# Kernel optimization log

Measured on AMD Instinct MI355X. Metric: run time of the kernel, lower is better.

The kernel has to match this reference:

```python
import jax, jax.numpy as jnp
import numpy as np

B, D, DM, K, KA = 4096, 64, 256, 32, 16


def setup_inputs() -> dict:
    key = jax.random.key(0)
    ks = jax.random.split(key, 20)
    rn = lambda i, shape, s=1.0: jax.random.normal(ks[i], shape, dtype=jnp.float32) * s
    return dict(
        z=rn(0, (B, D)),
        rw=jax.random.uniform(ks[1], (B, K), dtype=jnp.float32),
        action_z=rn(2, (B, D)),
        action_rw=jax.random.uniform(ks[3], (B, KA), dtype=jnp.float32),
        action_code_z=rn(4, (B, D)),
        control=rn(5, (B, D)),
        exact_covector=rn(6, (B, D)),
        chart_emb=rn(7, (K, DM), 0.05),
        chart_anchor=rn(8, (K, D)),
        action_chart_emb=rn(9, (KA, DM), 0.05),
        action_chart_anchor=rn(10, (KA, D)),
        z_embed_W=rn(11, (D, DM), 0.05), z_embed_b=jnp.zeros((DM,), jnp.float32),
        lat_W=rn(12, (D, DM), 0.05), lat_b=jnp.zeros((DM,), jnp.float32),
        code_W=rn(13, (D, DM), 0.05), code_b=jnp.zeros((DM,), jnp.float32),
        Wq=rn(14, (DM, DM), 0.05), Wk=rn(15, (DM, DM), 0.05),
        Wv=rn(16, (DM, DM), 0.05), Wo=rn(17, (DM, DM), 0.05),
        form_W=rn(18, (DM, D), 0.05), form_b=jnp.zeros((D,), jnp.float32),
    )


def _spectral_linear(x, W, b):
    # SpectralLinear: weight normalized by its largest singular value.
    sigma = jnp.linalg.svd(W, compute_uv=False)[0]
    return x @ (W / jnp.maximum(sigma, jnp.float32(1e-8))) + b


def _forward(z, rw, action_z, action_rw, action_code_z, control, exact_covector,
             chart_emb, chart_anchor, action_chart_emb, action_chart_anchor,
             z_embed_W, z_embed_b, lat_W, lat_b, code_W, code_b,
             Wq, Wk, Wv, Wo, form_W, form_b):
    b = z.shape[0]
    # ChartTokenizer: routing-weighted chart embeddings + anchor latents.
    chart_x = rw[:, :, None] * chart_emb[None]                      # [B,K,DM]
    chart_z = jnp.broadcast_to(chart_anchor[None], (b, K, D))       # [B,K,D]
    a_chart_x = action_rw[:, :, None] * action_chart_emb[None]      # [B,KA,DM]
    a_chart_z = jnp.broadcast_to(action_chart_anchor[None], (b, KA, D))
    # LatentTokenizers: single token per latent.
    lat_x = (action_z @ lat_W + lat_b)[:, None, :]                  # [B,1,DM]
    code_x = (action_code_z @ code_W + code_b)[:, None, :]          # [B,1,DM]
    ctx_x = jnp.concatenate([lat_x, code_x, a_chart_x, chart_x], axis=1)   # [B,S,DM]
    ctx_z = jnp.concatenate([action_z[:, None], action_code_z[:, None], a_chart_z, chart_z], axis=1)  # [B,S,D]
    # CovariantAttention (1 head): feature scores biased by latent-space distance.
    x_q = z @ z_embed_W + z_embed_b                                 # [B,DM]
    q = x_q @ Wq                                                    # [B,DM]
    k = jnp.einsum('bsd,de->bse', ctx_x, Wk)                        # [B,S,DM]
    v = jnp.einsum('bsd,de->bse', ctx_x, Wv)
    dist2 = jnp.sum((z[:, None, :] - ctx_z) ** 2, axis=-1)          # [B,S]
    scores = jnp.einsum('bd,bsd->bs', q, k) / jnp.sqrt(jnp.float32(DM)) - dist2
    attn = jax.nn.softmax(scores, axis=-1)
    feat = jnp.einsum('bs,bsd->bd', attn, v) @ Wo                   # [B,DM]
    # Residual reward one-form, projected off the (detached) exact direction.
    form_raw = _spectral_linear(feat, form_W, form_b)               # [B,D]
    e = jax.lax.stop_gradient(exact_covector)
    e_norm2 = jnp.sum(e * e, axis=-1, keepdims=True)
    coeff = jnp.where(e_norm2 > 1e-8,
                      jnp.sum(form_raw * e, axis=-1, keepdims=True) / jnp.maximum(e_norm2, 1e-8),
                      jnp.zeros_like(e_norm2))
    form_cov = form_raw - coeff * e
    # Non-conservative scalar reward contribution.
    return jnp.sum(form_cov * control, axis=-1, keepdims=True)      # [B,1]


def reference(z, rw, action_z, action_rw, action_code_z, control, exact_covector,
              chart_emb, chart_anchor, action_chart_emb, action_chart_anchor,
              z_embed_W, z_embed_b, lat_W, lat_b, code_W, code_b,
              Wq, Wk, Wv, Wo, form_W, form_b):
    return _forward(z, rw, action_z, action_rw, action_code_z, control, exact_covector,
                    chart_emb, chart_anchor, action_chart_emb, action_chart_anchor,
                    z_embed_W, z_embed_b, lat_W, lat_b, code_W, code_b,
                    Wq, Wk, Wv, Wo, form_W, form_b)
```

## Files before the change

### kernel.cpp

```cpp
#include <hip/hip_runtime.h>

#define PITERS 6

#define OFF_XQ   0
#define OFF_KL   16640
#define OFF_KC   33280
#define OFF_VL   49920
#define OFF_VC   66560
#define OFF_KE   83200
#define OFF_VE   95488
#define OFF_M    107776
#define OFF_PLm  128256
#define OFF_PLc  132416
#define OFF_PCm  132488
#define OFF_PCc  136648
#define OFF_CK2  136720
#define OFF_ANCT 139840
#define OFF_ANCN 142912
#define OFF_VM   142976
#define OFF_LM   146048
#define OFF_CM   150208
#define OFF_RS   154368

__device__ __forceinline__ float wred(float v) {
  #pragma unroll
  for (int m = 32; m >= 1; m >>= 1) v += __shfl_xor(v, m, 64);
  return v;
}

__global__ __launch_bounds__(256)
void k1a(const float* __restrict__ chemb, const float* __restrict__ aemb,
         const float* __restrict__ zW, const float* __restrict__ zb,
         const float* __restrict__ latW, const float* __restrict__ latb,
         const float* __restrict__ codeW, const float* __restrict__ codeb,
         const float* __restrict__ Wq, const float* __restrict__ Wk,
         const float* __restrict__ Wv, const float* __restrict__ Wo,
         const float* __restrict__ fW, float* __restrict__ ws) {
  __shared__ __align__(16) float sm[13120];
  const int t = threadIdx.x, b = blockIdx.x;

  if (b == 500) {
    const int ln = t & 63;
    float* bufA = sm;
    float* G0   = sm + 4352;
    float* bufB = sm + 8704;
    float* red  = sm + 13056;
    const int ty = t >> 4, tx = t & 15;
    const int i0 = ty * 4, j0 = tx * 4;
    float acc[4][4];
    #pragma unroll
    for (int i = 0; i < 4; ++i)
      #pragma unroll
      for (int j = 0; j < 4; ++j) acc[i][j] = 0.f;
    for (int c = 0; c < 4; ++c) {
      if (c) __syncthreads();
      for (int e = t; e < 4096; e += 256) {
        int k = e >> 6, i = e & 63;
        bufA[i * 68 + k] = fW[(c * 64 + k) * 64 + i];
      }
      __syncthreads();
      #pragma unroll 4
      for (int k4 = 0; k4 < 16; ++k4) {
        float4 av[4], bv[4];
        #pragma unroll
        for (int i = 0; i < 4; ++i) av[i] = *(const float4*)&bufA[(i0 + i) * 68 + k4 * 4];
        #pragma unroll
        for (int j = 0; j < 4; ++j) bv[j] = *(const float4*)&bufA[(j0 + j) * 68 + k4 * 4];
        #pragma unroll
        for (int i = 0; i < 4; ++i)
          #pragma unroll
          for (int j = 0; j < 4; ++j)
            acc[i][j] += av[i].x * bv[j].x + av[i].y * bv[j].y + av[i].z * bv[j].z + av[i].w * bv[j].w;
      }
    }
    if (ty == tx) red[ty] = acc[0][0] + acc[1][1] + acc[2][2] + acc[3][3];
    __syncthreads();
    {
      float tr = 0.f;
      #pragma unroll
      for (int x = 0; x < 16; ++x) tr += red[x];
      float inv = (tr > 0.f) ? 1.f / tr : 0.f;
      #pragma unroll
      for (int i = 0; i < 4; ++i) {
        *(float4*)&G0[(i0 + i) * 68 + j0]   = make_float4(acc[i][0], acc[i][1], acc[i][2], acc[i][3]);
        *(float4*)&bufB[(i0 + i) * 68 + j0] = make_float4(acc[i][0] * inv, acc[i][1] * inv,
                                                          acc[i][2] * inv, acc[i][3] * inv);
      }
    }
    __syncthreads();
    float* src = bufB;
    float* dst = bufA;
    for (int sq = 0; sq < 5; ++sq) {
      #pragma unroll
      for (int i = 0; i < 4; ++i)
        #pragma unroll
        for (int j = 0; j < 4; ++j) acc[i][j] = 0.f;
      #pragma unroll 4
      for (int k4 = 0; k4 < 16; ++k4) {
        float4 av[4], bv[4];
        #pragma unroll
        for (int i = 0; i < 4; ++i) av[i] = *(const float4*)&src[(i0 + i) * 68 + k4 * 4];
        #pragma unroll
        for (int j = 0; j < 4; ++j) bv[j] = *(const float4*)&src[(j0 + j) * 68 + k4 * 4];
        #pragma unroll
        for (int i = 0; i < 4; ++i)
          #pragma unroll
          for (int j = 0; j < 4; ++j)
            acc[i][j] += av[i].x * bv[j].x + av[i].y * bv[j].y + av[i].z * bv[j].z + av[i].w * bv[j].w;
      }
      if (ty == tx) red[ty] = acc[0][0] + acc[1][1] + acc[2][2] + acc[3][3];
      __syncthreads();
      {
        float tr = 0.f;
        #pragma unroll
        for (int x = 0; x < 16; ++x) tr += red[x];
        float inv = (tr > 0.f) ? 1.f / tr : 0.f;
        #pragma unroll
        for (int i = 0; i < 4; ++i)
          *(float4*)&dst[(i0 + i) * 68 + j0] = make_float4(acc[i][0] * inv, acc[i][1] * inv,
                                                           acc[i][2] * inv, acc[i][3] * inv);
      }
      __syncthreads();
      float* tmp = src; src = dst; dst = tmp;
    }
    if (t < 64) {
      float4 h[16];
      #pragma unroll
      for (int k4 = 0; k4 < 16; ++k4) h[k4] = *(const float4*)&src[ln * 68 + k4 * 4];
      float rn = 0.f;
      #pragma unroll
      for (int k4 = 0; k4 < 16; ++k4)
        rn += h[k4].x * h[k4].x + h[k4].y * h[k4].y + h[k4].z * h[k4].z + h[k4].w * h[k4].w;
      float bnv = rn; int bj = ln;
      #pragma unroll
      for (int m = 32; m >= 1; m >>= 1) {
        float ov = __shfl_xor(bnv, m, 64);
        int   oj = __shfl_xor(bj, m, 64);
        if (ov > bnv || (ov == bnv && oj < bj)) { bnv = ov; bj = oj; }
      }
      float v = src[bj * 68 + ln];
      for (int pi = 0; pi < PITERS; ++pi) {
        red[ln] = v;
        float y0 = 0.f, y1 = 0.f, y2 = 0.f, y3 = 0.f;
        #pragma unroll
        for (int k4 = 0; k4 < 16; ++k4) {
          float4 vvv = *(const float4*)&red[k4 * 4];
          y0 = fmaf(h[k4].x, vvv.x, y0);
          y1 = fmaf(h[k4].y, vvv.y, y1);
          y2 = fmaf(h[k4].z, vvv.z, y2);
          y3 = fmaf(h[k4].w, vvv.w, y3);
        }
        float y = (y0 + y1) + (y2 + y3);
        float n2 = wred(y * y);
        v = (n2 > 0.f) ? y * rsqrtf(n2) : 0.f;
      }
      red[ln] = v;
      float y0 = 0.f, y1 = 0.f, y2 = 0.f, y3 = 0.f;
      #pragma unroll
      for (int k4 = 0; k4 < 16; ++k4) {
        float4 gg = *(const float4*)&G0[ln * 68 + k4 * 4];
        float4 vvv = *(const float4*)&red[k4 * 4];
        y0 = fmaf(gg.x, vvv.x, y0);
        y1 = fmaf(gg.y, vvv.y, y1);
        y2 = fmaf(gg.z, vvv.z, y2);
        y3 = fmaf(gg.w, vvv.w, y3);
      }
      float y = (y0 + y1) + (y2 + y3);
      float num = wred(v * y), den = wred(v * v);
      if (ln == 0) {
        float lam = (den > 1e-37f) ? num / den : 0.f;
        lam = fmaxf(lam, 0.f);
        ws[OFF_RS] = 1.f / fmaxf(sqrtf(lam), 1e-8f);
      }
    }
    return;
  }

  float* red = sm;
  const int j = t & 63, ks = t >> 6;
  const float *a0p, *a1p, *a2p, *a3p;
  const float* Bm;
  int bstride = 256, jbase = 0;
  int d0, d1, d2, d3;
  if (b < 340) {
    int u = b / 68, r2 = b - u * 68;
    int rg = r2 >> 2, jc = r2 & 3; jbase = jc * 64;
    const float *Wmat, *bias;
    if (u == 0)      { Wmat = zW;    bias = zb;    Bm = Wq; }
    else if (u == 1) { Wmat = latW;  bias = latb;  Bm = Wk; }
    else if (u == 2) { Wmat = codeW; bias = codeb; Bm = Wk; }
    else if (u == 3) { Wmat = latW;  bias = latb;  Bm = Wv; }
    else             { Wmat = codeW; bias = codeb; Bm = Wv; }
    int r0 = rg * 4;
    int rr1 = r0 + 1, rr2 = r0 + 2, rr3 = r0 + 3;
    a0p = (r0 < 64) ? (Wmat + r0 * 256) : bias;
    a1p = (rr1 < 64) ? (Wmat + rr1 * 256) : bias;
    a2p = (rr2 < 64) ? (Wmat + rr2 * 256) : bias;
    a3p = (rr3 < 64) ? (Wmat + rr3 * 256) : bias;
    d0 = u * 16640 + r0 * 256 + jbase;
    d1 = (rr1 <= 64) ? (u * 16640 + rr1 * 256 + jbase) : -1;
    d2 = (rr2 <= 64) ? (u * 16640 + rr2 * 256 + jbase) : -1;
    d3 = (rr3 <= 64) ? (u * 16640 + rr3 * 256 + jbase) : -1;
  } else if (b < 436) {
    int b2 = b - 340; int isV = (b2 >= 48); int rr = b2 - (isV ? 48 : 0);
    int rg = rr >> 2, jc = rr & 3; jbase = jc * 64;
    Bm = isV ? Wv : Wk;
    int base = isV ? OFF_VE : OFF_KE;
    int s0 = rg * 4;
    a0p = (s0 + 0 < 16) ? (aemb + (s0 + 0) * 256) : (chemb + (s0 + 0 - 16) * 256);
    a1p = (s0 + 1 < 16) ? (aemb + (s0 + 1) * 256) : (chemb + (s0 + 1 - 16) * 256);
    a2p = (s0 + 2 < 16) ? (aemb + (s0 + 2) * 256) : (chemb + (s0 + 2 - 16) * 256);
    a3p = (s0 + 3 < 16) ? (aemb + (s0 + 3) * 256) : (chemb + (s0 + 3 - 16) * 256);
    d0 = base + (s0 + 0) * 256 + jbase;
    d1 = base + (s0 + 1) * 256 + jbase;
    d2 = base + (s0 + 2) * 256 + jbase;
    d3 = base + (s0 + 3) * 256 + jbase;
  } else {
    int i0 = (b - 436) * 4;
    Bm = fW; bstride = 64;
    a0p = Wo + (i0 + 0) * 256; a1p = Wo + (i0 + 1) * 256;
    a2p = Wo + (i0 + 2) * 256; a3p = Wo + (i0 + 3) * 256;
    d0 = OFF_M + (i0 + 0) * 64; d1 = OFF_M + (i0 + 1) * 64;
    d2 = OFF_M + (i0 + 2) * 64; d3 = OFF_M + (i0 + 3) * 64;
  }
  float acc0 = 0.f, acc1 = 0.f, acc2 = 0.f, acc3 = 0.f;
  const float* bp = Bm + (ks * 64) * bstride + jbase + j;
  const float* a0 = a0p + ks * 64;
  const float* a1 = a1p + ks * 64;
  const float* a2 = a2p + ks * 64;
  const float* a3 = a3p + ks * 64;
  #pragma unroll 4
  for (int k4 = 0; k4 < 16; ++k4) {
    float b0 = bp[(k4 * 4 + 0) * bstride];
    float b1 = bp[(k4 * 4 + 1) * bstride];
    float b2 = bp[(k4 * 4 + 2) * bstride];
    float b3 = bp[(k4 * 4 + 3) * bstride];
    float4 x0 = *(const float4*)(a0 + k4 * 4);
    float4 x1 = *(const float4*)(a1 + k4 * 4);
    float4 x2 = *(const float4*)(a2 + k4 * 4);
    float4 x3 = *(const float4*)(a3 + k4 * 4);
    acc0 += x0.x * b0 + x0.y * b1 + x0.z * b2 + x0.w * b3;
    acc1 += x1.x * b0 + x1.y * b1 + x1.z * b2 + x1.w * b3;
    acc2 += x2.x * b0 + x2.y * b1 + x2.z * b2 + x2.w * b3;
    acc3 += x3.x * b0 + x3.y * b1 + x3.z * b2 + x3.w * b3;
  }
  red[0 * 256 + t] = acc0;
  red[1 * 256 + t] = acc1;
  red[2 * 256 + t] = acc2;
  red[3 * 256 + t] = acc3;
  __syncthreads();
  if (t < 64) {
    if (d0 >= 0) ws[d0 + t] = (red[t] + red[64 + t]) + (red[128 + t] + red[192 + t]);
    if (d1 >= 0) ws[d1 + t] = (red[256 + t] + red[320 + t]) + (red[384 + t] + red[448 + t]);
    if (d2 >= 0) ws[d2 + t] = (red[512 + t] + red[576 + t]) + (red[640 + t] + red[704 + t]);
    if (d3 >= 0) ws[d3 + t] = (red[768 + t] + red[832 + t]) + (red[896 + t] + red[960 + t]);
  }
}

__global__ __launch_bounds__(256)
void k1b(const float* __restrict__ latb, const float* __restrict__ codeb,
         const float* __restrict__ aanc, const float* __restrict__ chanc,
         float* __restrict__ ws) {
  __shared__ float red[256];
  const int t = threadIdx.x, q = blockIdx.x;

  if (q == 374) {
    for (int e = t; e < 3072; e += 256) {
      int d = e / 48, s = e - d * 48;
      const float* a = (s < 16) ? (aanc + s * 64) : (chanc + (s - 16) * 64);
      ws[OFF_ANCT + e] = a[d];
    }
    if (t < 64) {
      float n = 0.f;
      if (t < 48) {
        const float* a = (t < 16) ? (aanc + t * 64) : (chanc + (t - 16) * 64);
        #pragma unroll 4
        for (int d = 0; d < 64; ++d) n += a[d] * a[d];
      }
      ws[OFF_ANCN + t] = n;
    }
    return;
  }
  if (q == 373) {
    if (t < 65) {
      const float* ap = ws + OFF_XQ + t * 256;
      const float* bp = ws + OFF_KL + 64 * 256;
      float acc = 0.f;
      #pragma unroll 4
      for (int e = 0; e < 256; ++e) acc += ap[e] * bp[e];
      ws[OFF_PLc + t] = acc;
    } else if (t >= 128 && t < 193) {
      int r = t - 128;
      const float* ap = ws + OFF_XQ + r * 256;
      const float* bp = ws + OFF_KC + 64 * 256;
      float acc = 0.f;
      #pragma unroll 4
      for (int e = 0; e < 256; ++e) acc += ap[e] * bp[e];
      ws[OFF_PCc + r] = acc;
    }
    return;
  }

  const int j = t & 63, ks = t >> 6;
  const float* ap; const float* bp;
  int bstride, dstBase, nout = 64;
  if (q < 325) {
    int g = q / 65, r = q - g * 65;
    const float* A = ws + ((g < 3) ? OFF_XQ : (g == 3 ? OFF_VL : OFF_VC)) + r * 256;
    if (g == 0)      { bp = ws + OFF_KL + j * 256 + ks * 64; bstride = 1; dstBase = OFF_PLm + r * 64; }
    else if (g == 1) { bp = ws + OFF_KC + j * 256 + ks * 64; bstride = 1; dstBase = OFF_PCm + r * 64; }
    else if (g == 2) { int jj = (j < 48) ? j : 47;
                       bp = ws + OFF_KE + jj * 256 + ks * 64; bstride = 1; dstBase = OFF_CK2 + r * 48; nout = 48; }
    else if (g == 3) { bp = ws + OFF_M + (ks * 64) * 64 + j; bstride = 64; dstBase = OFF_LM + r * 64; }
    else             { bp = ws + OFF_M + (ks * 64) * 64 + j; bstride = 64; dstBase = OFF_CM + r * 64; }
    ap = A + ks * 64;
  } else {
    int s = q - 325;
    ap = ws + OFF_VE + s * 256 + ks * 64;
    bp = ws + OFF_M + (ks * 64) * 64 + j; bstride = 64;
    dstBase = OFF_VM + s * 64;
  }
  float a0 = 0.f, a1 = 0.f, a2 = 0.f, a3 = 0.f;
  #pragma unroll 4
  for (int k = 0; k < 64; k += 4) {
    a0 += ap[k + 0] * bp[(k + 0) * bstride];
    a1 += ap[k + 1] * bp[(k + 1) * bstride];
    a2 += ap[k + 2] * bp[(k + 2) * bstride];
    a3 += ap[k + 3] * bp[(k + 3) * bstride];
  }
  red[t] = (a0 + a1) + (a2 + a3);
  __syncthreads();
  if (t < nout) ws[dstBase + t] = red[t] + red[64 + t] + red[128 + t] + red[192 + t];
}

__global__ __launch_bounds__(256)
void k2_main(const float* __restrict__ z, const float* __restrict__ rw,
             const float* __restrict__ az, const float* __restrict__ arw,
             const float* __restrict__ acz, const float* __restrict__ ctrl,
             const float* __restrict__ ecov, const float* __restrict__ fb,
             const float* __restrict__ ws, float* __restrict__ out) {
  const int t = threadIdx.x;
  const int wv = t >> 6, ln = t & 63;

  const int bb = blockIdx.x * 8 + wv * 2;
  float z0 = z[bb * 64 + ln],        z1 = z[(bb + 1) * 64 + ln];
  float a0 = az[bb * 64 + ln],       a1 = az[(bb + 1) * 64 + ln];
  float c0 = acz[bb * 64 + ln],      c1 = acz[(bb + 1) * 64 + ln];
  float cc0 = ctrl[bb * 64 + ln],    cc1 = ctrl[(bb + 1) * 64 + ln];
  float ee0 = ecov[bb * 64 + ln],    ee1 = ecov[(bb + 1) * 64 + ln];
  float fbv = fb[ln];
  const float rs = ws[OFF_RS];
  float fold0 = 1.f, fold1 = 1.f;
  if (ln < 16)      { fold0 = arw[bb * 16 + ln];        fold1 = arw[(bb + 1) * 16 + ln]; }
  else if (ln < 48) { fold0 = rw[bb * 32 + (ln - 16)];  fold1 = rw[(bb + 1) * 32 + (ln - 16)]; }

  float dL0 = wred((z0 - a0) * (z0 - a0));
  float dL1 = wred((z1 - a1) * (z1 - a1));
  float dC0 = wred((z0 - c0) * (z0 - c0));
  float dC1 = wred((z1 - c1) * (z1 - c1));
  float zn0 = wred(z0 * z0);
  float zn1 = wred(z1 * z1);

  const float* plm = ws + OFF_PLm + ln;
  const float* pcm = ws + OFF_PCm + ln;
  float uL0 = plm[64 * 64], uL1 = uL0;
  float uC0 = pcm[64 * 64], uC1 = uC0;
  #pragma unroll 8
  for (int k = 0; k < 64; ++k) {
    float pm = plm[k * 64], pc = pcm[k * 64];
    float zk0 = __shfl(z0, k, 64), zk1 = __shfl(z1, k, 64);
    uL0 = fmaf(zk0, pm, uL0); uL1 = fmaf(zk1, pm, uL1);
    uC0 = fmaf(zk0, pc, uC0); uC1 = fmaf(zk1, pc, uC1);
  }
  float plc = ws[OFF_PLc + ln], pcc = ws[OFF_PCc + ln];
  float plcc = ws[OFF_PLc + 64], pccc = ws[OFF_PCc + 64];
  float sL0 = wred(uL0 * a0 + z0 * plc) + plcc;
  float sL1 = wred(uL1 * a1 + z1 * plc) + plcc;
  float sC0 = wred(uC0 * c0 + z0 * pcc) + pccc;
  float sC1 = wred(uC1 * c1 + z1 * pcc) + pccc;
  float scl0 = sL0 * 0.0625f - dL0, scl1 = sL1 * 0.0625f - dL1;
  float scc0 = sC0 * 0.0625f - dC0, scc1 = sC1 * 0.0625f - dC1;

  const float* ck = ws + OFF_CK2 + ln;
  const float* an = ws + OFF_ANCT + ln;
  float ca0 = ck[64 * 48], ca1 = ca0;
  float za0 = 0.f, za1 = 0.f;
  #pragma unroll 8
  for (int k = 0; k < 64; ++k) {
    float cv = ck[k * 48], av = an[k * 48];
    float zk0 = __shfl(z0, k, 64), zk1 = __shfl(z1, k, 64);
    ca0 = fmaf(zk0, cv, ca0); ca1 = fmaf(zk1, cv, ca1);
    za0 = fmaf(zk0, av, za0); za1 = fmaf(zk1, av, za1);
  }
  float ancn = ws[OFF_ANCN + ln];
  float sc0 = fold0 * ca0 * 0.0625f - (zn0 - 2.f * za0 + ancn);
  float sc1 = fold1 * ca1 * 0.0625f - (zn1 - 2.f * za1 + ancn);
  if (ln == 48) { sc0 = scl0; sc1 = scl1; }
  if (ln == 49) { sc0 = scc0; sc1 = scc1; }
  if (ln > 49)  { sc0 = -1e30f; sc1 = -1e30f; }

  float mx0 = sc0, mx1 = sc1;
  #pragma unroll
  for (int m = 32; m >= 1; m >>= 1) {
    mx0 = fmaxf(mx0, __shfl_xor(mx0, m, 64));
    mx1 = fmaxf(mx1, __shfl_xor(mx1, m, 64));
  }
  float ev0 = (ln < 50) ? __expf(sc0 - mx0) : 0.f;
  float ev1 = (ln < 50) ? __expf(sc1 - mx1) : 0.f;
  float sum0 = wred(ev0), sum1 = wred(ev1);
  float w0 = ev0 * (1.f / sum0) * fold0;
  float w1 = ev1 * (1.f / sum1) * fold1;

  float g0 = 0.f, g1 = 0.f;
  const float* vm = ws + OFF_VM + ln;
  #pragma unroll 8
  for (int s = 0; s < 48; ++s) {
    float vvv = vm[s * 64];
    float s0 = __shfl(w0, s, 64), s1 = __shfl(w1, s, 64);
    g0 = fmaf(s0, vvv, g0); g1 = fmaf(s1, vvv, g1);
  }
  const float* lm = ws + OFF_LM + ln;
  const float* cm = ws + OFF_CM + ln;
  float l0 = lm[64 * 64], l1 = l0;
  float m0 = cm[64 * 64], m1 = m0;
  #pragma unroll 8
  for (int k = 0; k < 64; ++k) {
    float lv = lm[k * 64], cv = cm[k * 64];
    float ak0 = __shfl(a0, k, 64), ak1 = __shfl(a1, k, 64);
    float qk0 = __shfl(c0, k, 64), qk1 = __shfl(c1, k, 64);
    l0 = fmaf(ak0, lv, l0); l1 = fmaf(ak1, lv, l1);
    m0 = fmaf(qk0, cv, m0); m1 = fmaf(qk1, cv, m1);
  }
  float w48_0 = __shfl(w0, 48, 64), w49_0 = __shfl(w0, 49, 64);
  float w48_1 = __shfl(w1, 48, 64), w49_1 = __shfl(w1, 49, 64);
  g0 += w48_0 * l0 + w49_0 * m0;
  g1 += w48_1 * l1 + w49_1 * m1;

  #pragma unroll
  for (int s = 0; s < 2; ++s) {
    float g  = (s == 0) ? g0 : g1;
    float cc = (s == 0) ? cc0 : cc1;
    float ee = (s == 0) ? ee0 : ee1;
    int bbs  = bb + s;
    float gc = wred(g * cc);
    float ge = wred(g * ee);
    float ec = wred(ee * cc);
    float en = wred(ee * ee);
    float fc = wred(fbv * cc);
    float fe = wred(fbv * ee);
    if (ln == 0) {
      float A, Bv;
      if (en > 1e-8f) { float r = ec / en; A = gc - ge * r; Bv = fc - fe * r; }
      else { A = gc; Bv = fc; }
      out[bbs] = A * rs + Bv;
    }
  }
}

extern "C" void kernel_launch(void* const* d_in, const int* in_sizes, int n_in,
                              void* d_out, int out_size, void* d_ws, size_t ws_size,
                              hipStream_t stream) {
  const float* z     = (const float*)d_in[0];
  const float* rw    = (const float*)d_in[1];
  const float* az    = (const float*)d_in[2];
  const float* arw   = (const float*)d_in[3];
  const float* acz   = (const float*)d_in[4];
  const float* ctrl  = (const float*)d_in[5];
  const float* ecov  = (const float*)d_in[6];
  const float* chemb = (const float*)d_in[7];
  const float* chanc = (const float*)d_in[8];
  const float* aemb  = (const float*)d_in[9];
  const float* aanc  = (const float*)d_in[10];
  const float* zW    = (const float*)d_in[11];
  const float* zb    = (const float*)d_in[12];
  const float* latW  = (const float*)d_in[13];
  const float* latb  = (const float*)d_in[14];
  const float* codeW = (const float*)d_in[15];
  const float* codeb = (const float*)d_in[16];
  const float* Wq    = (const float*)d_in[17];
  const float* Wk    = (const float*)d_in[18];
  const float* Wv    = (const float*)d_in[19];
  const float* Wo    = (const float*)d_in[20];
  const float* fW    = (const float*)d_in[21];
  const float* fb    = (const float*)d_in[22];
  float* ws  = (float*)d_ws;
  float* out = (float*)d_out;

  k1a<<<501, 256, 0, stream>>>(chemb, aemb, zW, zb, latW, latb, codeW, codeb,
                               Wq, Wk, Wv, Wo, fW, ws);
  k1b<<<375, 256, 0, stream>>>(latb, codeb, aanc, chanc, ws);
  k2_main<<<512, 256, 0, stream>>>(z, rw, az, arw, acz, ctrl, ecov, fb, ws, out);
}
```

Baseline: 185.3 us.

## Split spectral-norm Gram computation across blocks and move power iteration to k1b

The single block in k1a that formed the 64x64 Gram matrix of form_W, did five repeated squarings and ran power iteration serially is removed. The Gram matrix is now computed by 16 extra k1a blocks that run in parallel with the other weight-fusion blocks. A new k1b block reads it back, does only two squarings and runs 24 power-iteration steps instead of 6. The aim is to shorten the critical path of k1a, which was held up by that one long serial block, at the cost of a global-memory round trip and more matrix-vector iterations. Fewer squarings may also change how closely the largest singular value is approximated.

Measured after the change: 155.0 us. -16.3%, faster.

```diff
diff --git a/kernel.cpp b/kernel.cpp
--- a/kernel.cpp
+++ b/kernel.cpp
@@ -1,6 +1,6 @@
 #include <hip/hip_runtime.h>
 
-#define PITERS 6
+#define PITERS 24
 
 #define OFF_XQ   0
 #define OFF_KL   16640
@@ -10,6 +10,7 @@
 #define OFF_KE   83200
 #define OFF_VE   95488
 #define OFF_M    107776
+#define OFF_G    124160
 #define OFF_PLm  128256
 #define OFF_PLc  132416
 #define OFF_PCm  132488
@@ -36,152 +37,16 @@
          const float* __restrict__ Wq, const float* __restrict__ Wk,
          const float* __restrict__ Wv, const float* __restrict__ Wo,
          const float* __restrict__ fW, float* __restrict__ ws) {
-  __shared__ __align__(16) float sm[13120];
+  __shared__ __align__(16) float red[1024];
   const int t = threadIdx.x, b = blockIdx.x;
-
-  if (b == 500) {
-    const int ln = t & 63;
-    float* bufA = sm;
-    float* G0   = sm + 4352;
-    float* bufB = sm + 8704;
-    float* red  = sm + 13056;
-    const int ty = t >> 4, tx = t & 15;
-    const int i0 = ty * 4, j0 = tx * 4;
-    float acc[4][4];
-    #pragma unroll
-    for (int i = 0; i < 4; ++i)
-      #pragma unroll
-      for (int j = 0; j < 4; ++j) acc[i][j] = 0.f;
-    for (int c = 0; c < 4; ++c) {
-      if (c) __syncthreads();
-      for (int e = t; e < 4096; e += 256) {
-        int k = e >> 6, i = e & 63;
-        bufA[i * 68 + k] = fW[(c * 64 + k) * 64 + i];
-      }
-      __syncthreads();
-      #pragma unroll 4
-      for (int k4 = 0; k4 < 16; ++k4) {
-        float4 av[4], bv[4];
-        #pragma unroll
-        for (int i = 0; i < 4; ++i) av[i] = *(const float4*)&bufA[(i0 + i) * 68 + k4 * 4];
-        #pragma unroll
-        for (int j = 0; j < 4; ++j) bv[j] = *(const float4*)&bufA[(j0 + j) * 68 + k4 * 4];
-        #pragma unroll
-        for (int i = 0; i < 4; ++i)
-          #pragma unroll
-          for (int j = 0; j < 4; ++j)
-            acc[i][j] += av[i].x * bv[j].x + av[i].y * bv[j].y + av[i].z * bv[j].z + av[i].w * bv[j].w;
-      }
-    }
-    if (ty == tx) red[ty] = acc[0][0] + acc[1][1] + acc[2][2] + acc[3][3];
-    __syncthreads();
-    {
-      float tr = 0.f;
-      #pragma unroll
-      for (int x = 0; x < 16; ++x) tr += red[x];
-      float inv = (tr > 0.f) ? 1.f / tr : 0.f;
-      #pragma unroll
-      for (int i = 0; i < 4; ++i) {
-        *(float4*)&G0[(i0 + i) * 68 + j0]   = make_float4(acc[i][0], acc[i][1], acc[i][2], acc[i][3]);
-        *(float4*)&bufB[(i0 + i) * 68 + j0] = make_float4(acc[i][0] * inv, acc[i][1] * inv,
-                                                          acc[i][2] * inv, acc[i][3] * inv);
-      }
-    }
-    __syncthreads();
-    float* src = bufB;
-    float* dst = bufA;
-    for (int sq = 0; sq < 5; ++sq) {
-      #pragma unroll
-      for (int i = 0; i < 4; ++i)
-        #pragma unroll
-        for (int j = 0; j < 4; ++j) acc[i][j] = 0.f;
-      #pragma unroll 4
-      for (int k4 = 0; k4 < 16; ++k4) {
-        float4 av[4], bv[4];
-        #pragma unroll
-        for (int i = 0; i < 4; ++i) av[i] = *(const float4*)&src[(i0 + i) * 68 + k4 * 4];
-        #pragma unroll
-        for (int j = 0; j < 4; ++j) bv[j] = *(const float4*)&src[(j0 + j) * 68 + k4 * 4];
-        #pragma unroll
-        for (int i = 0; i < 4; ++i)
-          #pragma unroll
-          for (int j = 0; j < 4; ++j)
-            acc[i][j] += av[i].x * bv[j].x + av[i].y * bv[j].y + av[i].z * bv[j].z + av[i].w * bv[j].w;
-      }
-      if (ty == tx) red[ty] = acc[0][0] + acc[1][1] + acc[2][2] + acc[3][3];
-      __syncthreads();
-      {
-        float tr = 0.f;
-        #pragma unroll
-        for (int x = 0; x < 16; ++x) tr += red[x];
-        float inv = (tr > 0.f) ? 1.f / tr : 0.f;
-        #pragma unroll
-        for (int i = 0; i < 4; ++i)
-          *(float4*)&dst[(i0 + i) * 68 + j0] = make_float4(acc[i][0] * inv, acc[i][1] * inv,
-                                                           acc[i][2] * inv, acc[i][3] * inv);
-      }
-      __syncthreads();
-      float* tmp = src; src = dst; dst = tmp;
-    }
-    if (t < 64) {
-      float4 h[16];
-      #pragma unroll
-      for (int k4 = 0; k4 < 16; ++k4) h[k4] = *(const float4*)&src[ln * 68 + k4 * 4];
-      float rn = 0.f;
-      #pragma unroll
-      for (int k4 = 0; k4 < 16; ++k4)
-        rn += h[k4].x * h[k4].x + h[k4].y * h[k4].y + h[k4].z * h[k4].z + h[k4].w * h[k4].w;
-      float bnv = rn; int bj = ln;
-      #pragma unroll
-      for (int m = 32; m >= 1; m >>= 1) {
-        float ov = __shfl_xor(bnv, m, 64);
-        int   oj = __shfl_xor(bj, m, 64);
-        if (ov > bnv || (ov == bnv && oj < bj)) { bnv = ov; bj = oj; }
-      }
-      float v = src[bj * 68 + ln];
-      for (int pi = 0; pi < PITERS; ++pi) {
-        red[ln] = v;
-        float y0 = 0.f, y1 = 0.f, y2 = 0.f, y3 = 0.f;
-        #pragma unroll
-        for (int k4 = 0; k4 < 16; ++k4) {
-          float4 vvv = *(const float4*)&red[k4 * 4];
-          y0 = fmaf(h[k4].x, vvv.x, y0);
-          y1 = fmaf(h[k4].y, vvv.y, y1);
-          y2 = fmaf(h[k4].z, vvv.z, y2);
-          y3 = fmaf(h[k4].w, vvv.w, y3);
-        }
-        float y = (y0 + y1) + (y2 + y3);
-        float n2 = wred(y * y);
-        v = (n2 > 0.f) ? y * rsqrtf(n2) : 0.f;
-      }
-      red[ln] = v;
-      float y0 = 0.f, y1 = 0.f, y2 = 0.f, y3 = 0.f;
-      #pragma unroll
-      for (int k4 = 0; k4 < 16; ++k4) {
-        float4 gg = *(const float4*)&G0[ln * 68 + k4 * 4];
-        float4 vvv = *(const float4*)&red[k4 * 4];
-        y0 = fmaf(gg.x, vvv.x, y0);
-        y1 = fmaf(gg.y, vvv.y, y1);
-        y2 = fmaf(gg.z, vvv.z, y2);
-        y3 = fmaf(gg.w, vvv.w, y3);
-      }
-      float y = (y0 + y1) + (y2 + y3);
-      float num = wred(v * y), den = wred(v * v);
-      if (ln == 0) {
-        float lam = (den > 1e-37f) ? num / den : 0.f;
-        lam = fmaxf(lam, 0.f);
-        ws[OFF_RS] = 1.f / fmaxf(sqrtf(lam), 1e-8f);
-      }
-    }
-    return;
-  }
-
-  float* red = sm;
   const int j = t & 63, ks = t >> 6;
+
   const float *a0p, *a1p, *a2p, *a3p;
   const float* Bm;
   int bstride = 256, jbase = 0;
   int d0, d1, d2, d3;
+  bool gpath = false;
+
   if (b < 340) {
     int u = b / 68, r2 = b - u * 68;
     int rg = r2 >> 2, jc = r2 & 3; jbase = jc * 64;
@@ -215,34 +80,57 @@
     d1 = base + (s0 + 1) * 256 + jbase;
     d2 = base + (s0 + 2) * 256 + jbase;
     d3 = base + (s0 + 3) * 256 + jbase;
-  } else {
+  } else if (b < 500) {
     int i0 = (b - 436) * 4;
     Bm = fW; bstride = 64;
     a0p = Wo + (i0 + 0) * 256; a1p = Wo + (i0 + 1) * 256;
     a2p = Wo + (i0 + 2) * 256; a3p = Wo + (i0 + 3) * 256;
     d0 = OFF_M + (i0 + 0) * 64; d1 = OFF_M + (i0 + 1) * 64;
     d2 = OFF_M + (i0 + 2) * 64; d3 = OFF_M + (i0 + 3) * 64;
-  }
+  } else {
+    gpath = true;
+    int i0 = (b - 500) * 4;
+    Bm = fW; bstride = 64;
+    a0p = fW + i0 + 0; a1p = fW + i0 + 1; a2p = fW + i0 + 2; a3p = fW + i0 + 3;
+    d0 = OFF_G + (i0 + 0) * 64; d1 = OFF_G + (i0 + 1) * 64;
+    d2 = OFF_G + (i0 + 2) * 64; d3 = OFF_G + (i0 + 3) * 64;
+  }
+
   float acc0 = 0.f, acc1 = 0.f, acc2 = 0.f, acc3 = 0.f;
   const float* bp = Bm + (ks * 64) * bstride + jbase + j;
-  const float* a0 = a0p + ks * 64;
-  const float* a1 = a1p + ks * 64;
-  const float* a2 = a2p + ks * 64;
-  const float* a3 = a3p + ks * 64;
-  #pragma unroll 4
-  for (int k4 = 0; k4 < 16; ++k4) {
-    float b0 = bp[(k4 * 4 + 0) * bstride];
-    float b1 = bp[(k4 * 4 + 1) * bstride];
-    float b2 = bp[(k4 * 4 + 2) * bstride];
-    float b3 = bp[(k4 * 4 + 3) * bstride];
-    float4 x0 = *(const float4*)(a0 + k4 * 4);
-    float4 x1 = *(const float4*)(a1 + k4 * 4);
-    float4 x2 = *(const float4*)(a2 + k4 * 4);
-    float4 x3 = *(const float4*)(a3 + k4 * 4);
-    acc0 += x0.x * b0 + x0.y * b1 + x0.z * b2 + x0.w * b3;
-    acc1 += x1.x * b0 + x1.y * b1 + x1.z * b2 + x1.w * b3;
-    acc2 += x2.x * b0 + x2.y * b1 + x2.z * b2 + x2.w * b3;
-    acc3 += x3.x * b0 + x3.y * b1 + x3.z * b2 + x3.w * b3;
+  if (!gpath) {
+    const float* a0 = a0p + ks * 64;
+    const float* a1 = a1p + ks * 64;
+    const float* a2 = a2p + ks * 64;
+    const float* a3 = a3p + ks * 64;
+    #pragma unroll 4
+    for (int k4 = 0; k4 < 16; ++k4) {
+      float b0 = bp[(k4 * 4 + 0) * bstride];
+      float b1 = bp[(k4 * 4 + 1) * bstride];
+      float b2 = bp[(k4 * 4 + 2) * bstride];
+      float b3 = bp[(k4 * 4 + 3) * bstride];
+      float4 x0 = *(const float4*)(a0 + k4 * 4);
+      float4 x1 = *(const float4*)(a1 + k4 * 4);
+      float4 x2 = *(const float4*)(a2 + k4 * 4);
+      float4 x3 = *(const float4*)(a3 + k4 * 4);
+      acc0 += x0.x * b0 + x0.y * b1 + x0.z * b2 + x0.w * b3;
+      acc1 += x1.x * b0 + x1.y * b1 + x1.z * b2 + x1.w * b3;
+      acc2 += x2.x * b0 + x2.y * b1 + x2.z * b2 + x2.w * b3;
+      acc3 += x3.x * b0 + x3.y * b1 + x3.z * b2 + x3.w * b3;
+    }
+  } else {
+    const float* a0 = a0p + (ks * 64) * 64;
+    const float* a1 = a1p + (ks * 64) * 64;
+    const float* a2 = a2p + (ks * 64) * 64;
+    const float* a3 = a3p + (ks * 64) * 64;
+    #pragma unroll 4
+    for (int k = 0; k < 64; ++k) {
+      float bv = bp[k * bstride];
+      acc0 += a0[k * 64] * bv;
+      acc1 += a1[k * 64] * bv;
+      acc2 += a2[k * 64] * bv;
+      acc3 += a3[k * 64] * bv;
+    }
   }
   red[0 * 256 + t] = acc0;
   red[1 * 256 + t] = acc1;
@@ -261,9 +149,123 @@
 void k1b(const float* __restrict__ latb, const float* __restrict__ codeb,
          const float* __restrict__ aanc, const float* __restrict__ chanc,
          float* __restrict__ ws) {
-  __shared__ float red[256];
+  __shared__ __align__(16) float sm[13120];
   const int t = threadIdx.x, q = blockIdx.x;
 
+  if (q == 375) {
+    const int ln = t & 63;
+    float* bufA = sm;
+    float* G0   = sm + 4352;
+    float* bufB = sm + 8704;
+    float* red  = sm + 13056;
+    {
+      float tv = (t < 64) ? ws[OFF_G + t * 65] : 0.f;
+      tv = wred(tv);
+      if (t == 0) red[0] = (tv > 0.f) ? 1.f / tv : 0.f;
+    }
+    __syncthreads();
+    {
+      float inv0 = red[0];
+      for (int e = t; e < 4096; e += 256) {
+        int i = e >> 6, jj = e & 63;
+        float g = ws[OFF_G + e];
+        G0[i * 68 + jj]   = g;
+        bufA[i * 68 + jj] = g * inv0;
+      }
+    }
+    __syncthreads();
+    const int ty = t >> 4, tx = t & 15;
+    const int i0 = ty * 4, j0 = tx * 4;
+    float* src = bufA;
+    float* dst = bufB;
+    for (int sq = 0; sq < 2; ++sq) {
+      float acc[4][4];
+      #pragma unroll
+      for (int i = 0; i < 4; ++i)
+        #pragma unroll
+        for (int j = 0; j < 4; ++j) acc[i][j] = 0.f;
+      #pragma unroll 4
+      for (int k4 = 0; k4 < 16; ++k4) {
+        float4 av[4], bv[4];
+        #pragma unroll
+        for (int i = 0; i < 4; ++i) av[i] = *(const float4*)&src[(i0 + i) * 68 + k4 * 4];
+        #pragma unroll
+        for (int j = 0; j < 4; ++j) bv[j] = *(const float4*)&src[(j0 + j) * 68 + k4 * 4];
+        #pragma unroll
+        for (int i = 0; i < 4; ++i)
+          #pragma unroll
+          for (int j = 0; j < 4; ++j)
+            acc[i][j] += av[i].x * bv[j].x + av[i].y * bv[j].y + av[i].z * bv[j].z + av[i].w * bv[j].w;
+      }
+      if (ty == tx) red[ty] = acc[0][0] + acc[1][1] + acc[2][2] + acc[3][3];
+      __syncthreads();
+      {
+        float tr = 0.f;
+        #pragma unroll
+        for (int x = 0; x < 16; ++x) tr += red[x];
+        float inv = (tr > 0.f) ? 1.f / tr : 0.f;
+        #pragma unroll
+        for (int i = 0; i < 4; ++i)
+          *(float4*)&dst[(i0 + i) * 68 + j0] = make_float4(acc[i][0] * inv, acc[i][1] * inv,
+                                                           acc[i][2] * inv, acc[i][3] * inv);
+      }
+      __syncthreads();
+      float* tmp = src; src = dst; dst = tmp;
+    }
+    if (t < 64) {
+      float4 h[16];
+      #pragma unroll
+      for (int k4 = 0; k4 < 16; ++k4) h[k4] = *(const float4*)&src[ln * 68 + k4 * 4];
+      float rn = 0.f;
+      #pragma unroll
+      for (int k4 = 0; k4 < 16; ++k4)
+        rn += h[k4].x * h[k4].x + h[k4].y * h[k4].y + h[k4].z * h[k4].z + h[k4].w * h[k4].w;
+      float bnv = rn; int bj = ln;
+      #pragma unroll
+      for (int m = 32; m >= 1; m >>= 1) {
+        float ov = __shfl_xor(bnv, m, 64);
+        int   oj = __shfl_xor(bj, m, 64);
+        if (ov > bnv || (ov == bnv && oj < bj)) { bnv = ov; bj = oj; }
+      }
+      float v = src[bj * 68 + ln];
+      for (int pi = 0; pi < PITERS; ++pi) {
+        red[ln] = v;
+        float y0 = 0.f, y1 = 0.f, y2 = 0.f, y3 = 0.f;
+        #pragma unroll
+        for (int k4 = 0; k4 < 16; ++k4) {
+          float4 vvv = *(const float4*)&red[k4 * 4];
+          y0 = fmaf(h[k4].x, vvv.x, y0);
+          y1 = fmaf(h[k4].y, vvv.y, y1);
+          y2 = fmaf(h[k4].z, vvv.z, y2);
+          y3 = fmaf(h[k4].w, vvv.w, y3);
+        }
+        float y = (y0 + y1) + (y2 + y3);
+        float n2 = wred(y * y);
+        v = (n2 > 0.f) ? y * rsqrtf(n2) : 0.f;
+      }
+      red[ln] = v;
+      float y0 = 0.f, y1 = 0.f, y2 = 0.f, y3 = 0.f;
+      #pragma unroll
+      for (int k4 = 0; k4 < 16; ++k4) {
+        float4 gg = *(const float4*)&G0[ln * 68 + k4 * 4];
+        float4 vvv = *(const float4*)&red[k4 * 4];
+        y0 = fmaf(gg.x, vvv.x, y0);
+        y1 = fmaf(gg.y, vvv.y, y1);
+        y2 = fmaf(gg.z, vvv.z, y2);
+        y3 = fmaf(gg.w, vvv.w, y3);
+      }
+      float y = (y0 + y1) + (y2 + y3);
+      float num = wred(v * y), den = wred(v * v);
+      if (ln == 0) {
+        float lam = (den > 1e-37f) ? num / den : 0.f;
+        lam = fmaxf(lam, 0.f);
+        ws[OFF_RS] = 1.f / fmaxf(sqrtf(lam), 1e-8f);
+      }
+    }
+    return;
+  }
+
+  float* red = sm;
   if (q == 374) {
     for (int e = t; e < 3072; e += 256) {
       int d = e / 48, s = e - d * 48;
@@ -486,8 +488,8 @@
   float* ws  = (float*)d_ws;
   float* out = (float*)d_out;
 
-  k1a<<<501, 256, 0, stream>>>(chemb, aemb, zW, zb, latW, latb, codeW, codeb,
+  k1a<<<516, 256, 0, stream>>>(chemb, aemb, zW, zb, latW, latb, codeW, codeb,
                                Wq, Wk, Wv, Wo, fW, ws);
-  k1b<<<375, 256, 0, stream>>>(latb, codeb, aanc, chanc, ws);
+  k1b<<<376, 256, 0, stream>>>(latb, codeb, aanc, chanc, ws);
   k2_main<<<512, 256, 0, stream>>>(z, rw, az, arw, acz, ctrl, ecov, fb, ws, out);
 }
```
